# Kernel optimization log

Hardware: AMD Instinct MI355X
Metric: run time of the kernel (lower is better)

The kernel has to match this reference:

```python
import jax, jax.numpy as jnp
import numpy as np

EPS = 1e-12  # F.normalize default eps

def l2norm(x, axis=1):
    n = jnp.sqrt(jnp.sum(x * x, axis=axis, keepdims=True))
    return x / jnp.maximum(n, EPS)

def setup_inputs() -> dict:
    key = jax.random.key(0)
    ks = jax.random.split(key, 8)
    N, C, H, W = 32, 1024, 28, 28
    D, K, OUT = 128, 64, 1024
    return {
        "x": jax.random.normal(ks[0], (N, C, H, W), dtype=jnp.float32),
        "Wpool": jax.random.normal(ks[1], (D, C), dtype=jnp.float32) * 0.02,
        "bpool": jax.random.normal(ks[2], (D,), dtype=jnp.float32) * 0.02,
        "Wconv": jax.random.normal(ks[3], (K, D), dtype=jnp.float32) * 0.1,
        "bconv": jax.random.normal(ks[4], (K,), dtype=jnp.float32) * 0.02,
        "centroids": jax.random.uniform(ks[5], (K, D), dtype=jnp.float32),
        "Wproj": jax.random.normal(ks[6], (OUT, K * D), dtype=jnp.float32) * 0.02,
        "bproj": jax.random.normal(ks[7], (OUT,), dtype=jnp.float32) * 0.02,
    }

def reference(x, Wpool, bpool, Wconv, bconv, centroids, Wproj, bproj):
    N, C, H, W = x.shape
    K, D = centroids.shape
    S = H * W
    # 1x1 conv channel pool: (N,C,H,W) -> (N,D,H,W)
    x = jnp.einsum('nchw,dc->ndhw', x, Wpool) + bpool[None, :, None, None]
    # descriptor-wise L2 norm over channel dim
    x = l2norm(x, axis=1)
    xf = x.reshape(N, D, S)                      # (N,D,S)
    # 1x1 conv -> soft assignment logits, softmax over clusters
    sa = jnp.einsum('nds,kd->nks', xf, Wconv) + bconv[None, :, None]
    sa = jax.nn.softmax(sa, axis=1)              # (N,K,S)
    # vlad[n,k,d] = sum_s sa[n,k,s]*(xf[n,d,s] - centroids[k,d])
    #            = (sa @ xf^T) - centroids * sum_s sa   (GEMM rewrite, same math)
    vlad = jnp.einsum('nks,nds->nkd', sa, xf) - centroids[None] * jnp.sum(sa, axis=-1)[:, :, None]
    vlad = l2norm(vlad, axis=1)                  # L2Norm over dim=1 (clusters)
    vlad = vlad.reshape(N, K * D)
    vlad = vlad @ Wproj.T + bproj
    return l2norm(vlad, axis=1)
```

## Files before the change

kernel.cpp:

```cpp
#include <hip/hip_runtime.h>
#include <math.h>

#define NB 32
#define CC 1024
#define SS 784
#define SP 832
#define DD 128
#define KK 64
#define OUTD 1024
#define KD 8192
#define NSPLIT 13
#define PSPLIT 32

#define OFF_XN    0
#define OFF_SA    (OFF_XN + NB*DD*SP*2)
#define OFF_WPK   (OFF_SA + NB*KK*SP*2)
#define OFF_WCK   (OFF_WPK + 32*8*64*8*2)
#define OFF_VLADP (OFF_WCK + 16*64*8*2)
#define OFF_SASUM (OFF_VLADP + NB*NSPLIT*KD*4)
#define OFF_VLADN (OFF_SASUM + NB*NSPLIT*KK*4)
#define OFF_OUTP  (OFF_VLADN + NB*KD*4)

typedef __attribute__((ext_vector_type(8))) short bf16x8;
typedef __attribute__((ext_vector_type(4))) float f32x4;
typedef __attribute__((ext_vector_type(4))) unsigned int u32x4;

__device__ __forceinline__ unsigned int pk_bf16(float a, float b) {
    unsigned int ua = __builtin_bit_cast(unsigned int, a);
    unsigned int ub = __builtin_bit_cast(unsigned int, b);
    ua += 0x7FFFu + ((ua >> 16) & 1u);
    ub += 0x7FFFu + ((ub >> 16) & 1u);
    return (ua >> 16) | (ub & 0xFFFF0000u);
}
__device__ __forceinline__ unsigned short f2bf(float a) {
    unsigned int ua = __builtin_bit_cast(unsigned int, a);
    ua += 0x7FFFu + ((ua >> 16) & 1u);
    return (unsigned short)(ua >> 16);
}
__device__ __forceinline__ float bf2f(unsigned short u) {
    unsigned int v = ((unsigned int)u) << 16;
    return __builtin_bit_cast(float, v);
}


__global__ __launch_bounds__(256)
void pack_weights(const float* __restrict__ Wpool, const float* __restrict__ Wconv,
                  unsigned short* __restrict__ Wpk, unsigned short* __restrict__ Wck)
{
    const int b = blockIdx.x;
    const int t = threadIdx.x;
    if (b < 8) {
        const int i = blockIdx.y;
        const int id = t + 256 * i;
        const int ktl = id >> 9;
        const int mt  = (id >> 6) & 7;
        const int l   = id & 63;
        const int lm = l & 15, quad = l >> 4;
        const int kt = b * 4 + ktl;
        const int d = mt * 16 + lm;
        const int cb = kt * 4 + quad;
        const int base_c = (cb >> 5) * 256 + ((cb >> 3) & 3) * 64 + (cb & 7);
        float v[8];
#pragma unroll
        for (int j = 0; j < 8; j++) v[j] = Wpool[(size_t)d * CC + base_c + 8 * j];
        unsigned int* dst = (unsigned int*)&Wpk[(size_t)((kt * 8 + mt) * 64 + l) * 8];
        dst[0] = pk_bf16(v[0], v[1]); dst[1] = pk_bf16(v[2], v[3]);
        dst[2] = pk_bf16(v[4], v[5]); dst[3] = pk_bf16(v[6], v[7]);
    } else if (blockIdx.y < 4) {
        const int i = blockIdx.y;
        const int id = t + 256 * i;
        const int tile = id >> 6;
        const int l = id & 63;
        const int lm = l & 15, quad = l >> 4;
        const int k = (tile >> 2) * 16 + lm;
        const int d = (tile & 3) * 32 + quad * 8;
        const float4 v0 = *(const float4*)&Wconv[(size_t)k * DD + d];
        const float4 v1 = *(const float4*)&Wconv[(size_t)k * DD + d + 4];
        unsigned int* dst = (unsigned int*)&Wck[(size_t)(tile * 64 + l) * 8];
        dst[0] = pk_bf16(v0.x, v0.y); dst[1] = pk_bf16(v0.z, v0.w);
        dst[2] = pk_bf16(v1.x, v1.y); dst[3] = pk_bf16(v1.z, v1.w);
    }
}

__global__ __launch_bounds__(256, 4)
void pool_norm_assign(const float* __restrict__ x, const unsigned short* __restrict__ Wpk,
                      const float* __restrict__ bpool, const unsigned short* __restrict__ Wck,
                      const float* __restrict__ bconv,
                      unsigned short* __restrict__ xn, unsigned short* __restrict__ sa)
{
    const int n  = blockIdx.y;
    const int s0 = blockIdx.x * 32;
    const int t  = threadIdx.x;
    const int l  = t & 63;
    const int w  = t >> 6;
    const int lm = l & 15;
    const int quad = l >> 4;

    __shared__ alignas(16) unsigned char smem[2 * 32 * 32 * 8 * 2 + 4 * 32 * 4];
    unsigned short* Bst0 = (unsigned short*)smem;
    unsigned short* Bst1 = Bst0 + 32 * 32 * 8;
    unsigned short* xnT  = Bst0;
    float* red  = (float*)(smem + 2 * 32 * 32 * 8 * 2);
    float* sums = red;

    unsigned short* xnp = xn + (size_t)n * DD * SP;
    unsigned short* sap = sa + (size_t)n * KK * SP;

    if (s0 >= SS) {
        const u32x4 z = (u32x4){0u, 0u, 0u, 0u};
#pragma unroll
        for (int pp = 0; pp < 2; pp++) {
            const int idx = t + 256 * pp;
            *(u32x4*)&xnp[(size_t)(idx >> 2) * SP + s0 + (idx & 3) * 8] = z;
        }
        *(u32x4*)&sap[(size_t)(t >> 2) * SP + s0 + (t & 3) * 8] = z;
        return;
    }

    const int r0 = (l >> 3) & 7;
    const int se = l & 7;
    int sc = s0 + se * 4;
    if (sc + 4 > SS) sc = s0 + (se & 3) * 4;
    const float* xw = x + (size_t)n * CC * SS + sc;
    const int crow0 = w * 64 + r0;

    f32x4 g[8];
#pragma unroll
    for (int j = 0; j < 8; j++)
        g[j] = *(const f32x4*)&xw[(size_t)(crow0 + j * 8) * SS];

    bf16x8 abuf[4][2];
#pragma unroll
    for (int p = 0; p < 4; p++)
#pragma unroll
        for (int i = 0; i < 2; i++)
            abuf[p][i] = *(const bf16x8*)&Wpk[(size_t)((p * 8 + w * 2 + i) * 64 + l) * 8];

    __builtin_amdgcn_sched_barrier(0);

#pragma unroll
    for (int ss = 0; ss < 4; ss++) {
        const int s = se * 4 + ss;
        const int sig = s ^ ((s >> 3) & 3);
        unsigned int* dst = (unsigned int*)&Bst0[(size_t)((w * 8 + r0) * 32 + sig) * 8];
        dst[0] = pk_bf16(g[0][ss], g[1][ss]); dst[1] = pk_bf16(g[2][ss], g[3][ss]);
        dst[2] = pk_bf16(g[4][ss], g[5][ss]); dst[3] = pk_bf16(g[6][ss], g[7][ss]);
    }
    __syncthreads();

    f32x4 acc[2][2];
#pragma unroll
    for (int i = 0; i < 2; i++)
#pragma unroll
        for (int h = 0; h < 2; h++) acc[i][h] = (f32x4){0.f, 0.f, 0.f, 0.f};

    for (int q = 0; q < 4; ++q) {
        if (q < 3) {
#pragma unroll
            for (int j = 0; j < 8; j++)
                g[j] = *(const f32x4*)&xw[(size_t)((q + 1) * 256 + crow0 + j * 8) * SS];
        }
        __builtin_amdgcn_sched_barrier(0);
        const unsigned short* Bq = (q & 1) ? Bst1 : Bst0;
#pragma unroll
        for (int ktq = 0; ktq < 8; ++ktq) {
            const int kt = q * 8 + ktq;
            const bf16x8 a0 = abuf[ktq & 3][0], a1 = abuf[ktq & 3][1];
            if (kt < 28) {
#pragma unroll
                for (int i = 0; i < 2; i++)
                    abuf[ktq & 3][i] = *(const bf16x8*)&Wpk[(size_t)(((kt + 4) * 8 + w * 2 + i) * 64 + l) * 8];
            }
#pragma unroll
            for (int h = 0; h < 2; h++) {
                const int s = h * 16 + lm;
                const int sig = s ^ ((s >> 3) & 3);
                const bf16x8 bf = *(const bf16x8*)&Bq[(size_t)((ktq * 4 + quad) * 32 + sig) * 8];
                acc[0][h] = __builtin_amdgcn_mfma_f32_16x16x32_bf16(a0, bf, acc[0][h], 0, 0, 0);
                acc[1][h] = __builtin_amdgcn_mfma_f32_16x16x32_bf16(a1, bf, acc[1][h], 0, 0, 0);
            }
        }
        __builtin_amdgcn_sched_barrier(0);
        if (q < 3) {
            unsigned short* Bn = ((q + 1) & 1) ? Bst1 : Bst0;
#pragma unroll
            for (int ss = 0; ss < 4; ss++) {
                const int s = se * 4 + ss;
                const int sig = s ^ ((s >> 3) & 3);
                unsigned int* dst = (unsigned int*)&Bn[(size_t)((w * 8 + r0) * 32 + sig) * 8];
                dst[0] = pk_bf16(g[0][ss], g[1][ss]); dst[1] = pk_bf16(g[2][ss], g[3][ss]);
                dst[2] = pk_bf16(g[4][ss], g[5][ss]); dst[3] = pk_bf16(g[6][ss], g[7][ss]);
            }
        }
        __syncthreads();
    }

    float vals[2][2][4];
    float ssq[2] = {0.f, 0.f};
#pragma unroll
    for (int i = 0; i < 2; i++)
#pragma unroll
        for (int h = 0; h < 2; h++)
#pragma unroll
            for (int r = 0; r < 4; r++) {
                const int d = (w * 2 + i) * 16 + quad * 4 + r;
                const float v = acc[i][h][r] + bpool[d];
                vals[i][h][r] = v; ssq[h] += v * v;
            }
#pragma unroll
    for (int h = 0; h < 2; h++) {
        ssq[h] += __shfl_xor(ssq[h], 16, 64);
        ssq[h] += __shfl_xor(ssq[h], 32, 64);
    }
    if (quad == 0) { red[w * 32 + lm] = ssq[0]; red[w * 32 + 16 + lm] = ssq[1]; }
    __syncthreads();
    float scale[2];
#pragma unroll
    for (int h = 0; h < 2; h++) {
        const int sl = h * 16 + lm;
        scale[h] = 1.f / fmaxf(sqrtf(red[0 * 32 + sl] + red[1 * 32 + sl] + red[2 * 32 + sl] + red[3 * 32 + sl]), 1e-12f);
    }
#pragma unroll
    for (int i = 0; i < 2; i++)
#pragma unroll
        for (int h = 0; h < 2; h++)
#pragma unroll
            for (int r = 0; r < 4; r++) {
                const int d = (w * 2 + i) * 16 + quad * 4 + r;
                const int sg = s0 + h * 16 + lm;
                const float v = vals[i][h][r] * scale[h];
                xnp[(size_t)d * SP + sg] = f2bf(v);
                xnT[(size_t)(((d >> 3) * 32) + h * 16 + lm) * 8 + (d & 7)] = f2bf(v);
            }
    __syncthreads();

    f32x4 acc2[2];
    acc2[0] = (f32x4){0.f, 0.f, 0.f, 0.f};
    acc2[1] = (f32x4){0.f, 0.f, 0.f, 0.f};
#pragma unroll
    for (int dsv = 0; dsv < 4; dsv++) {
        const bf16x8 afrag = *(const bf16x8*)&Wck[(size_t)((w * 4 + dsv) * 64 + l) * 8];
#pragma unroll
        for (int h = 0; h < 2; h++) {
            const bf16x8 bfrag = *(const bf16x8*)&xnT[(size_t)((dsv * 4 + quad) * 32 + h * 16 + lm) * 8];
            acc2[h] = __builtin_amdgcn_mfma_f32_16x16x32_bf16(afrag, bfrag, acc2[h], 0, 0, 0);
        }
    }
    float e[2][4]; float ps[2] = {0.f, 0.f};
#pragma unroll
    for (int h = 0; h < 2; h++)
#pragma unroll
        for (int r = 0; r < 4; r++) {
            const int k = w * 16 + quad * 4 + r;
            e[h][r] = expf(acc2[h][r] + bconv[k]);
            ps[h] += e[h][r];
        }
#pragma unroll
    for (int h = 0; h < 2; h++) {
        ps[h] += __shfl_xor(ps[h], 16, 64);
        ps[h] += __shfl_xor(ps[h], 32, 64);
    }
    if (quad == 0) { sums[w * 32 + lm] = ps[0]; sums[w * 32 + 16 + lm] = ps[1]; }
    __syncthreads();
#pragma unroll
    for (int h = 0; h < 2; h++) {
        const int sl = h * 16 + lm;
        const int sg = s0 + sl;
        const float inv = 1.f / (sums[0 * 32 + sl] + sums[1 * 32 + sl] + sums[2 * 32 + sl] + sums[3 * 32 + sl]);
        const bool val2 = sg < SS;
#pragma unroll
        for (int r = 0; r < 4; r++) {
            const int k = w * 16 + quad * 4 + r;
            sap[(size_t)k * SP + sg] = val2 ? f2bf(e[h][r] * inv) : (unsigned short)0;
        }
    }
}

__global__ __launch_bounds__(256)
void vlad_mfma(const unsigned short* __restrict__ xn, const unsigned short* __restrict__ sa,
               float* __restrict__ vladp, float* __restrict__ sasump)
{
    const int p = blockIdx.x;
    const int n = blockIdx.y;
    const int t = threadIdx.x;
    const int l = t & 63;
    const int w = t >> 6;
    const int kth = w & 1, nh = w >> 1;
    const int lm = l & 15, quad = l >> 4;

    const unsigned short* sap = sa + (size_t)n * KK * SP;
    const unsigned short* xnp = xn + (size_t)n * DD * SP;

    bf16x8 af[2][2], bfv[2][4];
#pragma unroll
    for (int st = 0; st < 2; st++) {
        const int sb = p * 64 + st * 32 + quad * 8;
#pragma unroll
        for (int j = 0; j < 2; j++)
            af[st][j] = *(const bf16x8*)&sap[(size_t)((kth * 2 + j) * 16 + lm) * SP + sb];
#pragma unroll
        for (int i = 0; i < 4; i++)
            bfv[st][i] = *(const bf16x8*)&xnp[(size_t)((nh * 4 + i) * 16 + lm) * SP + sb];
    }
    __builtin_amdgcn_sched_barrier(0);

    f32x4 acc[2][4];
#pragma unroll
    for (int j = 0; j < 2; j++)
#pragma unroll
        for (int i = 0; i < 4; i++) acc[j][i] = (f32x4){0.f, 0.f, 0.f, 0.f};

#pragma unroll
    for (int st = 0; st < 2; st++)
#pragma unroll
        for (int j = 0; j < 2; j++)
#pragma unroll
            for (int i = 0; i < 4; i++)
                acc[j][i] = __builtin_amdgcn_mfma_f32_16x16x32_bf16(af[st][j], bfv[st][i], acc[j][i], 0, 0, 0);

    float* vp = vladp + ((size_t)n * NSPLIT + p) * KD;
#pragma unroll
    for (int j = 0; j < 2; j++)
#pragma unroll
        for (int i = 0; i < 4; i++) {
            const int kq = (kth * 2 + j) * 4 + quad;
            const int d  = (nh * 4 + i) * 16 + lm;
            *(f32x4*)&vp[(size_t)(kq * DD + d) * 4] = acc[j][i];
        }

    if (t < KK) {
        const unsigned short* rp = &sap[(size_t)t * SP + p * 64];
        bf16x8 vv[8];
#pragma unroll
        for (int c8 = 0; c8 < 8; c8++) vv[c8] = *(const bf16x8*)&rp[c8 * 8];
        float sm = 0.f;
#pragma unroll
        for (int c8 = 0; c8 < 8; c8++)
#pragma unroll
            for (int j = 0; j < 8; j++) sm += bf2f((unsigned short)vv[c8][j]);
        sasump[((size_t)n * NSPLIT + p) * KK + t] = sm;
    }
}

__global__ __launch_bounds__(256)
void vlad_finish(const float* __restrict__ vladp, const float* __restrict__ sasump,
                 const float* __restrict__ centroids, float* __restrict__ vladn)
{
    const int dg = blockIdx.x;
    const int n  = blockIdx.y;
    const int t  = threadIdx.x;
    const int kq = t & 15;
    const int d  = dg * 16 + (t >> 4);

    __shared__ float sas[KK];
    if (t < KK) {
        float pv[NSPLIT];
#pragma unroll
        for (int p = 0; p < NSPLIT; p++) pv[p] = sasump[((size_t)n * NSPLIT + p) * KK + t];
        float sm = 0.f;
#pragma unroll
        for (int p = 0; p < NSPLIT; p++) sm += pv[p];
        sas[t] = sm;
    }
    __syncthreads();

    f32x4 pr[NSPLIT];
#pragma unroll
    for (int p = 0; p < NSPLIT; p++)
        pr[p] = *(const f32x4*)&vladp[((size_t)n * NSPLIT + p) * KD + (size_t)(kq * DD + d) * 4];
    __builtin_amdgcn_sched_barrier(0);

    f32x4 v = (f32x4){0.f, 0.f, 0.f, 0.f};
#pragma unroll
    for (int p = 0; p < NSPLIT; p++) v += pr[p];
#pragma unroll
    for (int r = 0; r < 4; r++)
        v[r] -= centroids[(size_t)(kq * 4 + r) * DD + d] * sas[kq * 4 + r];

    float ssq = v[0] * v[0] + v[1] * v[1] + v[2] * v[2] + v[3] * v[3];
    ssq += __shfl_xor(ssq, 1, 64);
    ssq += __shfl_xor(ssq, 2, 64);
    ssq += __shfl_xor(ssq, 4, 64);
    ssq += __shfl_xor(ssq, 8, 64);
    const float scale = 1.f / fmaxf(sqrtf(ssq), 1e-12f);

    float* vo = vladn + (size_t)n * KD;
#pragma unroll
    for (int r = 0; r < 4; r++)
        vo[(size_t)(kq * 4 + r) * DD + d] = v[r] * scale;
}

#define PROJ_ISSUE(L, KT) do {                                              \
    const int c_ = (KT) * 32;                                               \
    L[0] = *(const f32x4*)&wrow[c_];  L[1] = *(const f32x4*)&wrow[c_ + 4];  \
    L[2] = *(const f32x4*)&arow0[c_]; L[3] = *(const f32x4*)&arow0[c_ + 4]; \
    L[4] = *(const f32x4*)&arow1[c_]; L[5] = *(const f32x4*)&arow1[c_ + 4]; \
} while (0)

#define PROJ_STEP(L) do {                                                    \
    union { unsigned int u[4]; bf16x8 v; } ub, ua0, ua1;                     \
    ub.u[0]  = pk_bf16(L[0][0], L[0][1]); ub.u[1]  = pk_bf16(L[0][2], L[0][3]); \
    ub.u[2]  = pk_bf16(L[1][0], L[1][1]); ub.u[3]  = pk_bf16(L[1][2], L[1][3]); \
    ua0.u[0] = pk_bf16(L[2][0], L[2][1]); ua0.u[1] = pk_bf16(L[2][2], L[2][3]); \
    ua0.u[2] = pk_bf16(L[3][0], L[3][1]); ua0.u[3] = pk_bf16(L[3][2], L[3][3]); \
    ua1.u[0] = pk_bf16(L[4][0], L[4][1]); ua1.u[1] = pk_bf16(L[4][2], L[4][3]); \
    ua1.u[2] = pk_bf16(L[5][0], L[5][1]); ua1.u[3] = pk_bf16(L[5][2], L[5][3]); \
    acc[0] = __builtin_amdgcn_mfma_f32_16x16x32_bf16(ua0.v, ub.v, acc[0], 0, 0, 0); \
    acc[1] = __builtin_amdgcn_mfma_f32_16x16x32_bf16(ua1.v, ub.v, acc[1], 0, 0, 0); \
} while (0)

__global__ __launch_bounds__(256)
void proj_mfma(const float* __restrict__ vladn, const float* __restrict__ Wproj,
               float* __restrict__ outp)
{
    const int o0 = blockIdx.x * 64;
    const int c0 = blockIdx.y * (KD / PSPLIT);
    const int t  = threadIdx.x;
    const int l  = t & 63;
    const int w  = t >> 6;
    const int lm = l & 15, quad = l >> 4;
    const int o  = o0 + w * 16 + lm;

    const float* wrow  = &Wproj[(size_t)o * KD + c0 + quad * 8];
    const float* arow0 = &vladn[(size_t)lm * KD + c0 + quad * 8];
    const float* arow1 = &vladn[(size_t)(16 + lm) * KD + c0 + quad * 8];

    f32x4 acc[2];
    acc[0] = (f32x4){0.f, 0.f, 0.f, 0.f};
    acc[1] = (f32x4){0.f, 0.f, 0.f, 0.f};

    f32x4 LA[6], LB[6];
    PROJ_ISSUE(LA, 0);
#pragma unroll
    for (int kt = 0; kt < 8; kt += 2) {
        PROJ_ISSUE(LB, kt + 1);
        __builtin_amdgcn_sched_barrier(0);
        PROJ_STEP(LA);
        if (kt + 2 < 8) PROJ_ISSUE(LA, kt + 2);
        __builtin_amdgcn_sched_barrier(0);
        PROJ_STEP(LB);
    }

#pragma unroll
    for (int a = 0; a < 2; a++)
#pragma unroll
        for (int r = 0; r < 4; r++) {
            const int nn = a * 16 + quad * 4 + r;
            outp[((size_t)blockIdx.y * NB + nn) * OUTD + o] = acc[a][r];
        }
}

__global__ __launch_bounds__(256)
void final_norm_kernel(const float* __restrict__ outp, const float* __restrict__ bproj,
                       float* __restrict__ out)
{
    const int n = blockIdx.x;
    const int t = threadIdx.x;
    const int o4 = t * 4;

    float4 a = *(const float4*)&bproj[o4];
    f32x4 pr[16];
#pragma unroll
    for (int b = 0; b < 2; b++) {
#pragma unroll
        for (int i = 0; i < 16; i++)
            pr[i] = *(const f32x4*)&outp[((size_t)(b * 16 + i) * NB + n) * OUTD + o4];
        __builtin_amdgcn_sched_barrier(0);
#pragma unroll
        for (int i = 0; i < 16; i++) {
            a.x += pr[i][0]; a.y += pr[i][1]; a.z += pr[i][2]; a.w += pr[i][3];
        }
    }
    float ssp = a.x * a.x + a.y * a.y + a.z * a.z + a.w * a.w;
#pragma unroll
    for (int off = 32; off > 0; off >>= 1) ssp += __shfl_down(ssp, off, 64);
    __shared__ float rs[4];
    if ((t & 63) == 0) rs[t >> 6] = ssp;
    __syncthreads();
    const float total = rs[0] + rs[1] + rs[2] + rs[3];
    const float scale = 1.f / fmaxf(sqrtf(total), 1e-12f);
    float4 o;
    o.x = a.x * scale; o.y = a.y * scale; o.z = a.z * scale; o.w = a.w * scale;
    *(float4*)&out[(size_t)n * OUTD + o4] = o;
}

extern "C" void kernel_launch(void* const* d_in, const int* in_sizes, int n_in,
                              void* d_out, int out_size, void* d_ws, size_t ws_size,
                              hipStream_t stream)
{
    const float* x         = (const float*)d_in[0];
    const float* Wpool     = (const float*)d_in[1];
    const float* bpool     = (const float*)d_in[2];
    const float* Wconv     = (const float*)d_in[3];
    const float* bconv     = (const float*)d_in[4];
    const float* centroids = (const float*)d_in[5];
    const float* Wproj     = (const float*)d_in[6];
    const float* bproj     = (const float*)d_in[7];
    float* out = (float*)d_out;
    char*  wsb = (char*)d_ws;

    unsigned short* xn     = (unsigned short*)(wsb + OFF_XN);
    unsigned short* sa     = (unsigned short*)(wsb + OFF_SA);
    unsigned short* Wpk    = (unsigned short*)(wsb + OFF_WPK);
    unsigned short* Wck    = (unsigned short*)(wsb + OFF_WCK);
    float*          vladp  = (float*)(wsb + OFF_VLADP);
    float*          sasump = (float*)(wsb + OFF_SASUM);
    float*          vladn  = (float*)(wsb + OFF_VLADN);
    float*          outp   = (float*)(wsb + OFF_OUTP);

    pack_weights<<<dim3(9, 8), 256, 0, stream>>>(Wpool, Wconv, Wpk, Wck);
    pool_norm_assign<<<dim3(26, NB), 256, 0, stream>>>(x, Wpk, bpool, Wck, bconv, xn, sa);
    vlad_mfma<<<dim3(NSPLIT, NB), 256, 0, stream>>>(xn, sa, vladp, sasump);
    vlad_finish<<<dim3(DD / 16, NB), 256, 0, stream>>>(vladp, sasump, centroids, vladn);
    proj_mfma<<<dim3(OUTD / 64, PSPLIT), 256, 0, stream>>>(vladn, Wproj, outp);
    final_norm_kernel<<<dim3(NB), 256, 0, stream>>>(outp, bproj, out);
}
```

Measured before the change: 222.0 us.

## Fuse VLAD split-K GEMM with finish kernel and halve projection split

```diff
diff --git a/kernel.cpp b/kernel.cpp
--- a/kernel.cpp
+++ b/kernel.cpp
@@ -9,16 +9,13 @@
 #define KK 64
 #define OUTD 1024
 #define KD 8192
-#define NSPLIT 13
-#define PSPLIT 32
+#define PSPLIT 16
 
 #define OFF_XN    0
 #define OFF_SA    (OFF_XN + NB*DD*SP*2)
 #define OFF_WPK   (OFF_SA + NB*KK*SP*2)
 #define OFF_WCK   (OFF_WPK + 32*8*64*8*2)
-#define OFF_VLADP (OFF_WCK + 16*64*8*2)
-#define OFF_SASUM (OFF_VLADP + NB*NSPLIT*KD*4)
-#define OFF_VLADN (OFF_SASUM + NB*NSPLIT*KK*4)
+#define OFF_VLADN (OFF_WCK + 16*64*8*2)
 #define OFF_OUTP  (OFF_VLADN + NB*KD*4)
 
 typedef __attribute__((ext_vector_type(8))) short bf16x8;
@@ -277,117 +274,79 @@
 }
 
 __global__ __launch_bounds__(256)
-void vlad_mfma(const unsigned short* __restrict__ xn, const unsigned short* __restrict__ sa,
-               float* __restrict__ vladp, float* __restrict__ sasump)
-{
-    const int p = blockIdx.x;
-    const int n = blockIdx.y;
-    const int t = threadIdx.x;
-    const int l = t & 63;
-    const int w = t >> 6;
-    const int kth = w & 1, nh = w >> 1;
-    const int lm = l & 15, quad = l >> 4;
-
-    const unsigned short* sap = sa + (size_t)n * KK * SP;
-    const unsigned short* xnp = xn + (size_t)n * DD * SP;
-
-    bf16x8 af[2][2], bfv[2][4];
-#pragma unroll
-    for (int st = 0; st < 2; st++) {
-        const int sb = p * 64 + st * 32 + quad * 8;
-#pragma unroll
-        for (int j = 0; j < 2; j++)
-            af[st][j] = *(const bf16x8*)&sap[(size_t)((kth * 2 + j) * 16 + lm) * SP + sb];
-#pragma unroll
-        for (int i = 0; i < 4; i++)
-            bfv[st][i] = *(const bf16x8*)&xnp[(size_t)((nh * 4 + i) * 16 + lm) * SP + sb];
-    }
-    __builtin_amdgcn_sched_barrier(0);
-
-    f32x4 acc[2][4];
-#pragma unroll
-    for (int j = 0; j < 2; j++)
-#pragma unroll
-        for (int i = 0; i < 4; i++) acc[j][i] = (f32x4){0.f, 0.f, 0.f, 0.f};
-
-#pragma unroll
-    for (int st = 0; st < 2; st++)
-#pragma unroll
-        for (int j = 0; j < 2; j++)
-#pragma unroll
-            for (int i = 0; i < 4; i++)
-                acc[j][i] = __builtin_amdgcn_mfma_f32_16x16x32_bf16(af[st][j], bfv[st][i], acc[j][i], 0, 0, 0);
-
-    float* vp = vladp + ((size_t)n * NSPLIT + p) * KD;
-#pragma unroll
-    for (int j = 0; j < 2; j++)
-#pragma unroll
-        for (int i = 0; i < 4; i++) {
-            const int kq = (kth * 2 + j) * 4 + quad;
-            const int d  = (nh * 4 + i) * 16 + lm;
-            *(f32x4*)&vp[(size_t)(kq * DD + d) * 4] = acc[j][i];
-        }
-
-    if (t < KK) {
-        const unsigned short* rp = &sap[(size_t)t * SP + p * 64];
-        bf16x8 vv[8];
-#pragma unroll
-        for (int c8 = 0; c8 < 8; c8++) vv[c8] = *(const bf16x8*)&rp[c8 * 8];
-        float sm = 0.f;
-#pragma unroll
-        for (int c8 = 0; c8 < 8; c8++)
-#pragma unroll
-            for (int j = 0; j < 8; j++) sm += bf2f((unsigned short)vv[c8][j]);
-        sasump[((size_t)n * NSPLIT + p) * KK + t] = sm;
-    }
-}
-
-__global__ __launch_bounds__(256)
-void vlad_finish(const float* __restrict__ vladp, const float* __restrict__ sasump,
-                 const float* __restrict__ centroids, float* __restrict__ vladn)
+void vlad_full(const unsigned short* __restrict__ xn, const unsigned short* __restrict__ sa,
+               const float* __restrict__ centroids, float* __restrict__ vladn)
 {
     const int dg = blockIdx.x;
     const int n  = blockIdx.y;
     const int t  = threadIdx.x;
-    const int kq = t & 15;
-    const int d  = dg * 16 + (t >> 4);
+    const int l  = t & 63;
+    const int w  = t >> 6;
+    const int lm = l & 15, quad = l >> 4;
 
     __shared__ float sas[KK];
-    if (t < KK) {
-        float pv[NSPLIT];
-#pragma unroll
-        for (int p = 0; p < NSPLIT; p++) pv[p] = sasump[((size_t)n * NSPLIT + p) * KK + t];
-        float sm = 0.f;
-#pragma unroll
-        for (int p = 0; p < NSPLIT; p++) sm += pv[p];
-        sas[t] = sm;
-    }
-    __syncthreads();
-
-    f32x4 pr[NSPLIT];
-#pragma unroll
-    for (int p = 0; p < NSPLIT; p++)
-        pr[p] = *(const f32x4*)&vladp[((size_t)n * NSPLIT + p) * KD + (size_t)(kq * DD + d) * 4];
+    __shared__ float red[4][16];
+
+    const unsigned short* sap = sa + (size_t)n * KK * SP + (size_t)(w * 16 + lm) * SP + quad * 8;
+    const unsigned short* xnp = xn + (size_t)n * DD * SP + (size_t)(dg * 16 + lm) * SP + quad * 8;
+
+    f32x4 acc = (f32x4){0.f, 0.f, 0.f, 0.f};
+    float ssum = 0.f;
+
+    bf16x8 afA, bfA, afB, bfB;
+    afA = *(const bf16x8*)&sap[0];
+    bfA = *(const bf16x8*)&xnp[0];
+    afB = *(const bf16x8*)&sap[32];
+    bfB = *(const bf16x8*)&xnp[32];
     __builtin_amdgcn_sched_barrier(0);
 
-    f32x4 v = (f32x4){0.f, 0.f, 0.f, 0.f};
-#pragma unroll
-    for (int p = 0; p < NSPLIT; p++) v += pr[p];
-#pragma unroll
-    for (int r = 0; r < 4; r++)
-        v[r] -= centroids[(size_t)(kq * 4 + r) * DD + d] * sas[kq * 4 + r];
-
-    float ssq = v[0] * v[0] + v[1] * v[1] + v[2] * v[2] + v[3] * v[3];
-    ssq += __shfl_xor(ssq, 1, 64);
-    ssq += __shfl_xor(ssq, 2, 64);
-    ssq += __shfl_xor(ssq, 4, 64);
-    ssq += __shfl_xor(ssq, 8, 64);
-    const float scale = 1.f / fmaxf(sqrtf(ssq), 1e-12f);
+#pragma unroll
+    for (int st = 0; st < 26; st += 2) {
+        const bf16x8 a0 = afA, b0 = bfA;
+        if (st + 2 < 26) {
+            afA = *(const bf16x8*)&sap[(st + 2) * 32];
+            bfA = *(const bf16x8*)&xnp[(st + 2) * 32];
+        }
+        acc = __builtin_amdgcn_mfma_f32_16x16x32_bf16(a0, b0, acc, 0, 0, 0);
+#pragma unroll
+        for (int j = 0; j < 8; j++) ssum += bf2f((unsigned short)a0[j]);
+
+        const bf16x8 a1 = afB, b1 = bfB;
+        if (st + 3 < 26) {
+            afB = *(const bf16x8*)&sap[(st + 3) * 32];
+            bfB = *(const bf16x8*)&xnp[(st + 3) * 32];
+        }
+        acc = __builtin_amdgcn_mfma_f32_16x16x32_bf16(a1, b1, acc, 0, 0, 0);
+#pragma unroll
+        for (int j = 0; j < 8; j++) ssum += bf2f((unsigned short)a1[j]);
+    }
+
+    ssum += __shfl_xor(ssum, 16, 64);
+    ssum += __shfl_xor(ssum, 32, 64);
+    if (quad == 0) sas[w * 16 + lm] = ssum;
+    __syncthreads();
+
+    float v[4]; float ssq = 0.f;
+    const int d = dg * 16 + lm;
+#pragma unroll
+    for (int r = 0; r < 4; r++) {
+        const int k = w * 16 + quad * 4 + r;
+        v[r] = acc[r] - centroids[(size_t)k * DD + d] * sas[k];
+        ssq += v[r] * v[r];
+    }
+    ssq += __shfl_xor(ssq, 16, 64);
+    ssq += __shfl_xor(ssq, 32, 64);
+    if (quad == 0) red[w][lm] = ssq;
+    __syncthreads();
+    const float tot = red[0][lm] + red[1][lm] + red[2][lm] + red[3][lm];
+    const float scale = 1.f / fmaxf(sqrtf(tot), 1e-12f);
 
     float* vo = vladn + (size_t)n * KD;
 #pragma unroll
-    for (int r = 0; r < 4; r++)
-        vo[(size_t)(kq * 4 + r) * DD + d] = v[r] * scale;
+    for (int r = 0; r < 4; r++) {
+        const int k = w * 16 + quad * 4 + r;
+        vo[(size_t)k * DD + d] = v[r] * scale;
+    }
 }
 
 #define PROJ_ISSUE(L, KT) do {                                              \
@@ -432,11 +391,11 @@
     f32x4 LA[6], LB[6];
     PROJ_ISSUE(LA, 0);
 #pragma unroll
-    for (int kt = 0; kt < 8; kt += 2) {
+    for (int kt = 0; kt < 16; kt += 2) {
         PROJ_ISSUE(LB, kt + 1);
         __builtin_amdgcn_sched_barrier(0);
         PROJ_STEP(LA);
-        if (kt + 2 < 8) PROJ_ISSUE(LA, kt + 2);
+        if (kt + 2 < 16) PROJ_ISSUE(LA, kt + 2);
         __builtin_amdgcn_sched_barrier(0);
         PROJ_STEP(LB);
     }
@@ -459,17 +418,14 @@
     const int o4 = t * 4;
 
     float4 a = *(const float4*)&bproj[o4];
-    f32x4 pr[16];
-#pragma unroll
-    for (int b = 0; b < 2; b++) {
-#pragma unroll
-        for (int i = 0; i < 16; i++)
-            pr[i] = *(const f32x4*)&outp[((size_t)(b * 16 + i) * NB + n) * OUTD + o4];
-        __builtin_amdgcn_sched_barrier(0);
-#pragma unroll
-        for (int i = 0; i < 16; i++) {
-            a.x += pr[i][0]; a.y += pr[i][1]; a.z += pr[i][2]; a.w += pr[i][3];
-        }
+    f32x4 pr[PSPLIT];
+#pragma unroll
+    for (int i = 0; i < PSPLIT; i++)
+        pr[i] = *(const f32x4*)&outp[((size_t)i * NB + n) * OUTD + o4];
+    __builtin_amdgcn_sched_barrier(0);
+#pragma unroll
+    for (int i = 0; i < PSPLIT; i++) {
+        a.x += pr[i][0]; a.y += pr[i][1]; a.z += pr[i][2]; a.w += pr[i][3];
     }
     float ssp = a.x * a.x + a.y * a.y + a.z * a.z + a.w * a.w;
 #pragma unroll
@@ -503,15 +459,12 @@
     unsigned short* sa     = (unsigned short*)(wsb + OFF_SA);
     unsigned short* Wpk    = (unsigned short*)(wsb + OFF_WPK);
     unsigned short* Wck    = (unsigned short*)(wsb + OFF_WCK);
-    float*          vladp  = (float*)(wsb + OFF_VLADP);
-    float*          sasump = (float*)(wsb + OFF_SASUM);
     float*          vladn  = (float*)(wsb + OFF_VLADN);
     float*          outp   = (float*)(wsb + OFF_OUTP);
 
     pack_weights<<<dim3(9, 8), 256, 0, stream>>>(Wpool, Wconv, Wpk, Wck);
     pool_norm_assign<<<dim3(26, NB), 256, 0, stream>>>(x, Wpk, bpool, Wck, bconv, xn, sa);
-    vlad_mfma<<<dim3(NSPLIT, NB), 256, 0, stream>>>(xn, sa, vladp, sasump);
-    vlad_finish<<<dim3(DD / 16, NB), 256, 0, stream>>>(vladp, sasump, centroids, vladn);
+    vlad_full<<<dim3(DD / 16, NB), 256, 0, stream>>>(xn, sa, centroids, vladn);
     proj_mfma<<<dim3(OUTD / 64, PSPLIT), 256, 0, stream>>>(vladn, Wproj, outp);
     final_norm_kernel<<<dim3(NB), 256, 0, stream>>>(outp, bproj, out);
 }
```

Result: faster. 216.5 us, median of 2 (-2.5%).
